# Kernel tuning notes

Measured on AMD Instinct MI355X. Metric: run time of the kernel, lower is better.

The kernel has to match this reference:

```python
import jax, jax.numpy as jnp
import numpy as np
import math

H, W, R = 100, 100, 2          # BEV grid and neighbor range
K = (2 * R + 1) ** 2           # 25 spatial neighbors
C = 256                        # input_dim == hidden_dim
NH, DK = 8, 32                 # heads, head dim
T = 5                          # temporal history length
NEG = -1e10                    # mask fill value from the source


def build_neighbors():
    # Clamped (2R+1)x(2R+1) window per pixel (faithful to the intent of
    # generate_spatial_neighbors: edge pixels reuse the nearest interior window).
    hs = np.clip(np.arange(H), R, H - 1 - R)
    ws = np.clip(np.arange(W), R, W - 1 - R)
    off = np.arange(-R, R + 1)
    rows = hs[:, None] + off[None, :]                      # [H, 2R+1]
    cols = ws[:, None] + off[None, :]                      # [W, 2R+1]
    idx = rows[:, None, :, None] * W + cols[None, :, None, :]  # [H,W,2R+1,2R+1]
    return idx.reshape(H * W, K).astype(np.int32)


def setup_inputs() -> dict:
    key = jax.random.key(0)
    ks = jax.random.split(key, 40)
    N = H * W
    inp = {"x": jax.random.normal(ks[0], (N, T, C), jnp.float32)}
    i = 1
    for pfx in ("t", "s"):
        for nm in ("q", "k", "v", "o"):
            inp[f"{pfx}_W{nm}"] = jax.random.normal(ks[i], (C, C), jnp.float32) * 0.02; i += 1
            inp[f"{pfx}_b{nm}"] = jax.random.normal(ks[i], (C,), jnp.float32) * 0.02; i += 1
    inp["neighbors"] = jnp.asarray(build_neighbors())
    inp["tmask"] = jnp.ones((N, 1, T), jnp.int32)
    inp["smask"] = jnp.ones((N, 1, K), jnp.int32)
    return inp


def _heads(x, Wx, b):
    # x: [N, L, C] -> [N, NH, L, DK]
    N, L, _ = x.shape
    return (x @ Wx + b).reshape(N, L, NH, DK).transpose(0, 2, 1, 3)


def _attend(q, k, v, mask4):
    # q: [N,NH,Lq,DK], k/v: [N,NH,Lk,DK], mask4: [N,1,1,Lk]
    scores = jnp.einsum('nhqd,nhkd->nhqk', q, k) / math.sqrt(q.shape[-1])
    scores = jnp.where(mask4 == 0, NEG, scores)
    p = jax.nn.softmax(scores, axis=-1)
    return jnp.einsum('nhqk,nhkd->nhqd', p, v)


def _forward(x, t_Wq, t_bq, t_Wk, t_bk, t_Wv, t_bv, t_Wo, t_bo,
             s_Wq, s_bq, s_Wk, s_bk, s_Wv, s_bv, s_Wo, s_bo,
             neighbors, tmask, smask):
    N = x.shape[0]
    # ---- temporal aggregation (MultiHeadedAttention): latest frame attends history
    q_last = x[:, -1:, :]                                   # [N,1,C]
    q = _heads(q_last, t_Wq, t_bq)                          # [N,NH,1,DK]
    k = _heads(x, t_Wk, t_bk)                               # [N,NH,T,DK]
    v = _heads(x, t_Wv, t_bv)
    ctx = _attend(q, k, v, tmask[:, None, :, :])            # [N,NH,1,DK]
    h_t = ctx.transpose(0, 2, 1, 3).reshape(N, 1, C) @ t_Wo + t_bo  # [N,1,C]
    # ---- spatial neighbor attention (MultiHeadedAttention_spatial):
    # K/V are projected from the query features, then gathered by neighbor index.
    sq = _heads(h_t, s_Wq, s_bq)                            # [N,NH,1,DK]
    k1 = h_t[:, 0, :] @ s_Wk + s_bk                          # [N,C] per-pixel key token
    v1 = h_t[:, 0, :] @ s_Wv + s_bv                          # [N,C]
    kn = k1[neighbors].reshape(N, K, NH, DK).transpose(0, 2, 1, 3)  # [N,NH,K,DK]
    vn = v1[neighbors].reshape(N, K, NH, DK).transpose(0, 2, 1, 3)
    sctx = _attend(sq, kn, vn, smask[:, None, :, :])        # [N,NH,1,DK]
    out = sctx.transpose(0, 2, 1, 3).reshape(N, 1, C) @ s_Wo + s_bo  # [N,1,C]
    return out


def reference(x, t_Wq, t_bq, t_Wk, t_bk, t_Wv, t_bv, t_Wo, t_bo,
              s_Wq, s_bq, s_Wk, s_bk, s_Wv, s_bv, s_Wo, s_bo,
              neighbors, tmask, smask):
    return _forward(x, t_Wq, t_bq, t_Wk, t_bk, t_Wv, t_bv, t_Wo, t_bo,
                    s_Wq, s_bq, s_Wk, s_bk, s_Wv, s_bv, s_Wo, s_bo,
                    neighbors, tmask, smask)
```

## Files before the change

kernel.cpp:

```cpp
#include <hip/hip_runtime.h>

constexpr int TT = 5;
constexpr int KK = 25;
#define NEGV -1e10f

typedef _Float16 f16;
typedef __attribute__((ext_vector_type(8))) _Float16 f16x8;
typedef __attribute__((ext_vector_type(4))) _Float16 f16x4;
typedef __attribute__((ext_vector_type(4))) float f32x4;

__device__ __forceinline__ void gload16(const void* g, void* l) {
    __builtin_amdgcn_global_load_lds(
        (const __attribute__((address_space(1))) unsigned int*)g,
        (__attribute__((address_space(3))) unsigned int*)l, 16, 0, 0);
}

__device__ __forceinline__ int xcd_remap(int id, int G) {
    const int c = id & 7, j = id >> 3;
    const int q = G >> 3, r = G & 7;
    const int base = (c < r) ? c * (q + 1) : r * (q + 1) + (c - r) * q;
    return base + j;
}

struct PrepArgs { const float* W[8]; const float* b[8]; };

__global__ __launch_bounds__(256) void prep_w8(
    PrepArgs pa, f16* __restrict__ wt, float* __restrict__ bc)
{
    __shared__ float sT[64][65];
    const int z = blockIdx.z;
    const float* W = pa.W[z];
    f16* wh = wt + (size_t)z * 65536;
    const int t  = threadIdx.x;
    const int k0 = blockIdx.x * 64, n0 = blockIdx.y * 64;
    const int kk = t >> 2;
    #pragma unroll
    for (int c = 0; c < 4; ++c) {
        const int col = (t & 3) * 16 + c * 4;
        float4 v = *(const float4*)(W + (size_t)(k0 + kk) * 256 + n0 + col);
        sT[kk][col] = v.x; sT[kk][col + 1] = v.y; sT[kk][col + 2] = v.z; sT[kk][col + 3] = v.w;
    }
    __syncthreads();
    const int n = t >> 2, ks = (t & 3) * 16;
    f16* ph = wh + (size_t)(n0 + n) * 256 + k0 + ks;
    #pragma unroll
    for (int j0 = 0; j0 < 16; j0 += 8) {
        f16x8 vh;
        #pragma unroll
        for (int j = 0; j < 8; ++j) vh[j] = (f16)sT[ks + j0 + j][n];
        *(f16x8*)(ph + j0) = vh;
    }
    if (blockIdx.x == 0 && blockIdx.y == 0) bc[z * 256 + t] = pa.b[z][t];
}

__global__ __launch_bounds__(256) void cvt_x(
    const float* __restrict__ x, f16* __restrict__ xh, int n8)
{
    for (int i = blockIdx.x * 256 + threadIdx.x; i < n8; i += gridDim.x * 256) {
        const float4 a = ((const float4*)x)[2 * i];
        const float4 b = ((const float4*)x)[2 * i + 1];
        f16x8 o;
        o[0] = (f16)a.x; o[1] = (f16)a.y; o[2] = (f16)a.z; o[3] = (f16)a.w;
        o[4] = (f16)b.x; o[5] = (f16)b.y; o[6] = (f16)b.z; o[7] = (f16)b.w;
        *(f16x8*)(xh + (size_t)i * 8) = o;
    }
}

template<int BM, int OM>
__global__ __launch_bounds__(512, 4) void gemm_f16(
    const f16* __restrict__ A, int lda, int M,
    const f16* __restrict__ W, const float* __restrict__ bias,
    float* __restrict__ Cf, f16* __restrict__ Ch, int ldc,
    int GY, int G)
{
    constexpr int MF   = BM / 32;
    constexpr int ASEG = BM / 64;
    __shared__ f16 sA[2][BM * 64];
    __shared__ f16 sB[2][128 * 64];

    const int tid = threadIdx.x;
    const int l   = tid & 63, w = tid >> 6;
    const int l15 = l & 15, l4 = l >> 4;
    const int wm  = w >> 2, wn = w & 3;

    const int p  = xcd_remap(blockIdx.x, G);
    const int bm = (p / GY) * BM;
    const int bn = (p % GY) * 128;

    const int srow8 = l >> 3;
    const int scol  = ((l & 7) ^ srow8) * 8;
    size_t aoff[ASEG];
    #pragma unroll
    for (int j = 0; j < ASEG; ++j) {
        int r = bm + (w * ASEG + j) * 8 + srow8;
        if (r > M - 1) r = M - 1;
        aoff[j] = (size_t)r * lda + scol;
    }
    size_t boff[2];
    #pragma unroll
    for (int j = 0; j < 2; ++j)
        boff[j] = (size_t)(bn + (w * 2 + j) * 8 + srow8) * 256 + scol;

    f32x4 acc[MF][2];
    #pragma unroll
    for (int i = 0; i < MF; ++i)
        #pragma unroll
        for (int j = 0; j < 2; ++j) acc[i][j] = f32x4{0.f, 0.f, 0.f, 0.f};

    auto STAGE = [&](int buf, int k0) {
        #pragma unroll
        for (int j = 0; j < ASEG; ++j)
            gload16(A + aoff[j] + k0, &sA[buf][(w * ASEG + j) * 512]);
        #pragma unroll
        for (int j = 0; j < 2; ++j)
            gload16(W + boff[j] + k0, &sB[buf][(w * 2 + j) * 512]);
    };

    STAGE(0, 0);
    __syncthreads();

    const int swz = l15 & 7;
    #pragma unroll
    for (int t = 0; t < 4; ++t) {
        if (t < 3) STAGE((t + 1) & 1, (t + 1) * 64);

        f16x8 af[MF][2], bf[2][2];
        #pragma unroll
        for (int mf = 0; mf < MF; ++mf) {
            const int r = wm * (BM / 2) + mf * 16 + l15;
            #pragma unroll
            for (int ks = 0; ks < 2; ++ks)
                af[mf][ks] = *(const f16x8*)&sA[t & 1][r * 64 + (((ks * 4 + l4) ^ swz) * 8)];
        }
        #pragma unroll
        for (int nf = 0; nf < 2; ++nf) {
            const int r = wn * 32 + nf * 16 + l15;
            #pragma unroll
            for (int ks = 0; ks < 2; ++ks)
                bf[nf][ks] = *(const f16x8*)&sB[t & 1][r * 64 + (((ks * 4 + l4) ^ swz) * 8)];
        }
        #pragma unroll
        for (int mf = 0; mf < MF; ++mf)
            #pragma unroll
            for (int nf = 0; nf < 2; ++nf)
                #pragma unroll
                for (int ks = 0; ks < 2; ++ks)
                    acc[mf][nf] = __builtin_amdgcn_mfma_f32_16x16x32_f16(
                        af[mf][ks], bf[nf][ks], acc[mf][nf], 0, 0, 0);
        __syncthreads();
    }

    #pragma unroll
    for (int mf = 0; mf < MF; ++mf) {
        const int row0 = bm + wm * (BM / 2) + mf * 16 + l4 * 4;
        #pragma unroll
        for (int nf = 0; nf < 2; ++nf) {
            const int col = bn + wn * 32 + nf * 16 + l15;
            const float bs = bias[col];
            #pragma unroll
            for (int i = 0; i < 4; ++i) {
                const int row = row0 + i;
                if (row < M) {
                    const float v = acc[mf][nf][i] + bs;
                    const size_t o = (size_t)row * ldc + col;
                    if (OM == 0) Cf[o] = v;
                    else         Ch[o] = (f16)v;
                }
            }
        }
    }
}

__global__ __launch_bounds__(256) void attn_t(
    const f16* __restrict__ q, const f16* __restrict__ kv,
    const int* __restrict__ tmask, f16* __restrict__ ctx)
{
    const int tid = threadIdx.x;
    const int wv = tid >> 6, l = tid & 63;
    const int n = blockIdx.x * 4 + wv;
    const int col = ((l >> 3) * 32) + (l & 7) * 4;
    const float scale = 0.1767766952966369f;

    const f16x4 qv = *(const f16x4*)(q + (size_t)n * 256 + col);
    const float q0 = (float)qv[0], q1 = (float)qv[1], q2 = (float)qv[2], q3 = (float)qv[3];

    float m = -3.0e38f, lsum = 0.f;
    float a0 = 0.f, a1 = 0.f, a2 = 0.f, a3 = 0.f;
    #pragma unroll
    for (int t = 0; t < TT; ++t) {
        const size_t row = ((size_t)n * TT + t) * 512;
        const f16x4 kk = *(const f16x4*)(kv + row + col);
        const f16x4 vv = *(const f16x4*)(kv + row + 256 + col);
        float p = q0 * (float)kk[0] + q1 * (float)kk[1]
                + q2 * (float)kk[2] + q3 * (float)kk[3];
        p += __shfl_xor(p, 1);
        p += __shfl_xor(p, 2);
        p += __shfl_xor(p, 4);
        const float s  = (tmask[n * TT + t] == 0) ? NEGV : p * scale;
        const float mn = fmaxf(m, s);
        const float sc = exp2f((m - mn) * 1.44269504f);
        const float pe = exp2f((s - mn) * 1.44269504f);
        lsum = lsum * sc + pe;
        a0 = a0 * sc + pe * (float)vv[0];
        a1 = a1 * sc + pe * (float)vv[1];
        a2 = a2 * sc + pe * (float)vv[2];
        a3 = a3 * sc + pe * (float)vv[3];
        m = mn;
    }
    const float inv = 1.0f / lsum;
    f16x4 o;
    o[0] = (f16)(a0 * inv); o[1] = (f16)(a1 * inv);
    o[2] = (f16)(a2 * inv); o[3] = (f16)(a3 * inv);
    *(f16x4*)(ctx + (size_t)n * 256 + col) = o;
}

__global__ __launch_bounds__(256) void attn_s(
    const f16* __restrict__ sqkv, const int* __restrict__ nbrs,
    const int* __restrict__ smask, f16* __restrict__ sctx, int G)
{
    __shared__ int nbL[4 * KK];
    __shared__ int mkL[4 * KK];
    const int tid = threadIdx.x;
    const int nbase = xcd_remap(blockIdx.x, G) * 4;
    if (tid < 4 * KK) {
        nbL[tid] = nbrs[nbase * KK + tid];
        mkL[tid] = smask[nbase * KK + tid];
    }
    __syncthreads();

    const int wv = tid >> 6, l = tid & 63;
    const int n = nbase + wv;
    const int col = ((l >> 3) * 32) + (l & 7) * 4;
    const float scale = 0.1767766952966369f;

    const f16x4 qv = *(const f16x4*)(sqkv + (size_t)n * 768 + col);
    const float q0 = (float)qv[0], q1 = (float)qv[1], q2 = (float)qv[2], q3 = (float)qv[3];

    float m = -3.0e38f, lsum = 0.f;
    float a0 = 0.f, a1 = 0.f, a2 = 0.f, a3 = 0.f;
    #pragma unroll
    for (int j = 0; j < KK; ++j) {
        const size_t row = (size_t)nbL[wv * KK + j] * 768;
        const f16x4 kk = *(const f16x4*)(sqkv + row + 256 + col);
        const f16x4 vv = *(const f16x4*)(sqkv + row + 512 + col);
        float p = q0 * (float)kk[0] + q1 * (float)kk[1]
                + q2 * (float)kk[2] + q3 * (float)kk[3];
        p += __shfl_xor(p, 1);
        p += __shfl_xor(p, 2);
        p += __shfl_xor(p, 4);
        const float s  = (mkL[wv * KK + j] == 0) ? NEGV : p * scale;
        const float mn = fmaxf(m, s);
        const float sc = exp2f((m - mn) * 1.44269504f);
        const float pe = exp2f((s - mn) * 1.44269504f);
        lsum = lsum * sc + pe;
        a0 = a0 * sc + pe * (float)vv[0];
        a1 = a1 * sc + pe * (float)vv[1];
        a2 = a2 * sc + pe * (float)vv[2];
        a3 = a3 * sc + pe * (float)vv[3];
        m = mn;
    }
    const float inv = 1.0f / lsum;
    f16x4 o;
    o[0] = (f16)(a0 * inv); o[1] = (f16)(a1 * inv);
    o[2] = (f16)(a2 * inv); o[3] = (f16)(a3 * inv);
    *(f16x4*)(sctx + (size_t)n * 256 + col) = o;
}

extern "C" void kernel_launch(void* const* d_in, const int* in_sizes, int n_in,
                              void* d_out, int out_size, void* d_ws, size_t ws_size,
                              hipStream_t stream)
{
    const float* x = (const float*)d_in[0];
    const int* nbrs  = (const int*)d_in[17];
    const int* tmask = (const int*)d_in[18];
    const int* smask = (const int*)d_in[19];
    float* out = (float*)d_out;

    const int N  = in_sizes[0] / (TT * 256);
    const int MT = N * TT;

    f16* wt  = (f16*)d_ws;
    float* bc = (float*)(wt + (size_t)2048 * 256);
    f16* xh     = (f16*)(bc + 2048);
    f16* kvbuf  = xh + (size_t)MT * 256;
    f16* q16    = kvbuf + (size_t)MT * 512;
    f16* ctx    = q16 + (size_t)N * 256;
    f16* ht     = ctx + (size_t)N * 256;
    f16* sqkv16 = ht + (size_t)N * 256;
    f16* sctx   = sqkv16 + (size_t)N * 768;

    PrepArgs pa;
    pa.W[0] = (const float*)d_in[3];  pa.b[0] = (const float*)d_in[4];
    pa.W[1] = (const float*)d_in[5];  pa.b[1] = (const float*)d_in[6];
    pa.W[2] = (const float*)d_in[1];  pa.b[2] = (const float*)d_in[2];
    pa.W[3] = (const float*)d_in[7];  pa.b[3] = (const float*)d_in[8];
    pa.W[4] = (const float*)d_in[9];  pa.b[4] = (const float*)d_in[10];
    pa.W[5] = (const float*)d_in[11]; pa.b[5] = (const float*)d_in[12];
    pa.W[6] = (const float*)d_in[13]; pa.b[6] = (const float*)d_in[14];
    pa.W[7] = (const float*)d_in[15]; pa.b[7] = (const float*)d_in[16];
    prep_w8<<<dim3(4, 4, 8), 256, 0, stream>>>(pa, wt, bc);

    cvt_x<<<2048, 256, 0, stream>>>(x, xh, MT * 256 / 8);

    dim3 blk(512);
    const int GBM_T = (MT + 127) / 128;
    const int GBM_S = (N + 63) / 64;

    gemm_f16<128, 1><<<GBM_T * 4, blk, 0, stream>>>(
        xh, 256, MT, wt, bc, nullptr, kvbuf, 512, 4, GBM_T * 4);
    gemm_f16<64, 1><<<GBM_S * 2, blk, 0, stream>>>(
        xh + (TT - 1) * 256, TT * 256, N,
        wt + (size_t)512 * 256, bc + 512, nullptr, q16, 256, 2, GBM_S * 2);
    attn_t<<<N / 4, dim3(256), 0, stream>>>(q16, kvbuf, tmask, ctx);
    gemm_f16<64, 1><<<GBM_S * 2, blk, 0, stream>>>(
        ctx, 256, N, wt + (size_t)768 * 256, bc + 768,
        nullptr, ht, 256, 2, GBM_S * 2);
    gemm_f16<64, 1><<<GBM_S * 6, blk, 0, stream>>>(
        ht, 256, N, wt + (size_t)1024 * 256, bc + 1024,
        nullptr, sqkv16, 768, 6, GBM_S * 6);
    attn_s<<<N / 4, dim3(256), 0, stream>>>(sqkv16, nbrs, smask, sctx, N / 4);
    gemm_f16<64, 0><<<GBM_S * 2, blk, 0, stream>>>(
        sctx, 256, N, wt + (size_t)1792 * 256, bc + 1792,
        out, nullptr, 256, 2, GBM_S * 2);
}
```

Measured before the change: 227.1 us.

## Fold temporal output projection into spatial QKV weights and batch kernel launches

Precomputes the product of the temporal output projection and the spatial Q/K/V weights (plus the folded bias) inside the prep kernel, which removes the h_t GEMM and its intermediate buffer. Weight prep and x conversion are merged into one launch, and the KV and Q projection GEMMs share a single launch through a two-job dispatch. All GEMMs now use 128-row tiles. This cuts two launches and one full GEMM pass, in exchange for a small fp32 weight-product GEMM each call and different fp16 rounding of the combined weights.

```diff
diff --git a/kernel.cpp b/kernel.cpp
--- a/kernel.cpp
+++ b/kernel.cpp
@@ -22,60 +22,111 @@
     return base + j;
 }
 
-struct PrepArgs { const float* W[8]; const float* b[8]; };
-
-__global__ __launch_bounds__(256) void prep_w8(
-    PrepArgs pa, f16* __restrict__ wt, float* __restrict__ bc)
-{
-    __shared__ float sT[64][65];
-    const int z = blockIdx.z;
-    const float* W = pa.W[z];
-    f16* wh = wt + (size_t)z * 65536;
-    const int t  = threadIdx.x;
-    const int k0 = blockIdx.x * 64, n0 = blockIdx.y * 64;
-    const int kk = t >> 2;
-    #pragma unroll
-    for (int c = 0; c < 4; ++c) {
-        const int col = (t & 3) * 16 + c * 4;
-        float4 v = *(const float4*)(W + (size_t)(k0 + kk) * 256 + n0 + col);
-        sT[kk][col] = v.x; sT[kk][col + 1] = v.y; sT[kk][col + 2] = v.z; sT[kk][col + 3] = v.w;
-    }
-    __syncthreads();
-    const int n = t >> 2, ks = (t & 3) * 16;
-    f16* ph = wh + (size_t)(n0 + n) * 256 + k0 + ks;
-    #pragma unroll
-    for (int j0 = 0; j0 < 16; j0 += 8) {
-        f16x8 vh;
-        #pragma unroll
-        for (int j = 0; j < 8; ++j) vh[j] = (f16)sT[ks + j0 + j][n];
-        *(f16x8*)(ph + j0) = vh;
-    }
-    if (blockIdx.x == 0 && blockIdx.y == 0) bc[z * 256 + t] = pa.b[z][t];
-}
-
-__global__ __launch_bounds__(256) void cvt_x(
+struct PrepAll {
+    const float* Wt[4]; const float* bt[4];
+    const float* tWo;   const float* tbo;
+    const float* sW[3]; const float* sb[3];
+};
+
+__global__ __launch_bounds__(256) void prep_all(
+    PrepAll pp, f16* __restrict__ wt, float* __restrict__ bc,
+    f16* __restrict__ wc, float* __restrict__ bcs,
     const float* __restrict__ x, f16* __restrict__ xh, int n8)
 {
-    for (int i = blockIdx.x * 256 + threadIdx.x; i < n8; i += gridDim.x * 256) {
-        const float4 a = ((const float4*)x)[2 * i];
-        const float4 b = ((const float4*)x)[2 * i + 1];
-        f16x8 o;
-        o[0] = (f16)a.x; o[1] = (f16)a.y; o[2] = (f16)a.z; o[3] = (f16)a.w;
-        o[4] = (f16)b.x; o[5] = (f16)b.y; o[6] = (f16)b.z; o[7] = (f16)b.w;
-        *(f16x8*)(xh + (size_t)i * 8) = o;
-    }
-}
-
-template<int BM, int OM>
-__global__ __launch_bounds__(512, 4) void gemm_f16(
-    const f16* __restrict__ A, int lda, int M,
-    const f16* __restrict__ W, const float* __restrict__ bias,
-    float* __restrict__ Cf, f16* __restrict__ Ch, int ldc,
-    int GY, int G)
-{
-    constexpr int MF   = BM / 32;
-    constexpr int ASEG = BM / 64;
-    __shared__ f16 sA[2][BM * 64];
+    const int bid = blockIdx.x, t = threadIdx.x;
+
+    if (bid < 64) {
+        __shared__ float sT[64][65];
+        const int z = bid >> 4, sub = bid & 15;
+        const int k0 = (sub >> 2) * 64, n0 = (sub & 3) * 64;
+        const float* W = pp.Wt[z];
+        f16* wh = wt + (size_t)z * 65536;
+        const int kk = t >> 2;
+        #pragma unroll
+        for (int c = 0; c < 4; ++c) {
+            const int col = (t & 3) * 16 + c * 4;
+            float4 v = *(const float4*)(W + (size_t)(k0 + kk) * 256 + n0 + col);
+            sT[kk][col] = v.x; sT[kk][col + 1] = v.y;
+            sT[kk][col + 2] = v.z; sT[kk][col + 3] = v.w;
+        }
+        __syncthreads();
+        const int n = t >> 2, ks = (t & 3) * 16;
+        f16* ph = wh + (size_t)(n0 + n) * 256 + k0 + ks;
+        #pragma unroll
+        for (int j0 = 0; j0 < 16; j0 += 8) {
+            f16x8 vh;
+            #pragma unroll
+            for (int j = 0; j < 8; ++j) vh[j] = (f16)sT[ks + j0 + j][n];
+            *(f16x8*)(ph + j0) = vh;
+        }
+        if (sub == 0) bc[z * 256 + t] = pp.bt[z][t];
+    } else if (bid < 112) {
+        const int cb = bid - 64;
+        const int m0 = (cb / 12) * 64;
+        const int nt = cb % 12;
+        const int sel = nt >> 2;
+        const int nc0 = (nt & 3) * 64;
+        const float* Amat = pp.tWo;
+        const float* Bmat = pp.sW[sel];
+        __shared__ float sa[16][68];
+        __shared__ float sbm[16][64];
+        const int tm = t >> 4, tn = t & 15;
+        const int r = t >> 2, cA = (t & 3) << 2;
+        const int kB = t >> 4, jB = (t & 15) << 2;
+        float acc[4][4] = {};
+        for (int c0 = 0; c0 < 256; c0 += 16) {
+            float4 a4 = *(const float4*)(Amat + (size_t)(m0 + r) * 256 + c0 + cA);
+            float4 b4 = *(const float4*)(Bmat + (size_t)(c0 + kB) * 256 + nc0 + jB);
+            __syncthreads();
+            sa[cA + 0][r] = a4.x; sa[cA + 1][r] = a4.y;
+            sa[cA + 2][r] = a4.z; sa[cA + 3][r] = a4.w;
+            *(float4*)(&sbm[kB][jB]) = b4;
+            __syncthreads();
+            #pragma unroll
+            for (int k = 0; k < 16; ++k) {
+                float4 a = *(const float4*)(&sa[k][tm * 4]);
+                float4 b = *(const float4*)(&sbm[k][tn * 4]);
+                acc[0][0] += a.x * b.x; acc[0][1] += a.x * b.y; acc[0][2] += a.x * b.z; acc[0][3] += a.x * b.w;
+                acc[1][0] += a.y * b.x; acc[1][1] += a.y * b.y; acc[1][2] += a.y * b.z; acc[1][3] += a.y * b.w;
+                acc[2][0] += a.z * b.x; acc[2][1] += a.z * b.y; acc[2][2] += a.z * b.z; acc[2][3] += a.z * b.w;
+                acc[3][0] += a.w * b.x; acc[3][1] += a.w * b.y; acc[3][2] += a.w * b.z; acc[3][3] += a.w * b.w;
+            }
+        }
+        const int ng0 = nt * 64 + tn * 4;
+        #pragma unroll
+        for (int i = 0; i < 4; ++i)
+            #pragma unroll
+            for (int j = 0; j < 4; ++j)
+                wc[(size_t)(ng0 + j) * 256 + m0 + tm * 4 + i] = (f16)acc[i][j];
+    } else if (bid == 112) {
+        #pragma unroll
+        for (int rgn = 0; rgn < 3; ++rgn) {
+            const float* B = pp.sW[rgn];
+            float a = 0.f;
+            for (int c = 0; c < 256; ++c) a += pp.tbo[c] * B[(size_t)c * 256 + t];
+            bcs[rgn * 256 + t] = a + pp.sb[rgn][t];
+        }
+    } else {
+        for (int i = (bid - 113) * 256 + t; i < n8; i += 2048 * 256) {
+            const float4 a = ((const float4*)x)[2 * i];
+            const float4 b = ((const float4*)x)[2 * i + 1];
+            f16x8 o;
+            o[0] = (f16)a.x; o[1] = (f16)a.y; o[2] = (f16)a.z; o[3] = (f16)a.w;
+            o[4] = (f16)b.x; o[5] = (f16)b.y; o[6] = (f16)b.z; o[7] = (f16)b.w;
+            *(f16x8*)(xh + (size_t)i * 8) = o;
+        }
+    }
+}
+
+struct GJob {
+    const f16* A; const f16* W; const float* bias;
+    f16* C16; float* C32;
+    int lda, M, ldc, GY, nblk;
+};
+
+__global__ __launch_bounds__(512, 4) void gemm_f16(GJob j0, GJob j1, int G)
+{
+    __shared__ f16 sA[2][128 * 64];
     __shared__ f16 sB[2][128 * 64];
 
     const int tid = threadIdx.x;
@@ -83,37 +134,41 @@
     const int l15 = l & 15, l4 = l >> 4;
     const int wm  = w >> 2, wn = w & 3;
 
-    const int p  = xcd_remap(blockIdx.x, G);
-    const int bm = (p / GY) * BM;
-    const int bn = (p % GY) * 128;
+    int p = xcd_remap(blockIdx.x, G);
+    const bool first = (p < j0.nblk);
+    const GJob jb = first ? j0 : j1;
+    if (!first) p -= j0.nblk;
+
+    const int bm = (p / jb.GY) * 128;
+    const int bn = (p % jb.GY) * 128;
 
     const int srow8 = l >> 3;
     const int scol  = ((l & 7) ^ srow8) * 8;
-    size_t aoff[ASEG];
-    #pragma unroll
-    for (int j = 0; j < ASEG; ++j) {
-        int r = bm + (w * ASEG + j) * 8 + srow8;
-        if (r > M - 1) r = M - 1;
-        aoff[j] = (size_t)r * lda + scol;
+    size_t aoff[2];
+    #pragma unroll
+    for (int j = 0; j < 2; ++j) {
+        int r = bm + (w * 2 + j) * 8 + srow8;
+        if (r > jb.M - 1) r = jb.M - 1;
+        aoff[j] = (size_t)r * jb.lda + scol;
     }
     size_t boff[2];
     #pragma unroll
     for (int j = 0; j < 2; ++j)
         boff[j] = (size_t)(bn + (w * 2 + j) * 8 + srow8) * 256 + scol;
 
-    f32x4 acc[MF][2];
-    #pragma unroll
-    for (int i = 0; i < MF; ++i)
+    f32x4 acc[4][2];
+    #pragma unroll
+    for (int i = 0; i < 4; ++i)
         #pragma unroll
         for (int j = 0; j < 2; ++j) acc[i][j] = f32x4{0.f, 0.f, 0.f, 0.f};
 
     auto STAGE = [&](int buf, int k0) {
         #pragma unroll
-        for (int j = 0; j < ASEG; ++j)
-            gload16(A + aoff[j] + k0, &sA[buf][(w * ASEG + j) * 512]);
-        #pragma unroll
         for (int j = 0; j < 2; ++j)
-            gload16(W + boff[j] + k0, &sB[buf][(w * 2 + j) * 512]);
+            gload16(jb.A + aoff[j] + k0, &sA[buf][(w * 2 + j) * 512]);
+        #pragma unroll
+        for (int j = 0; j < 2; ++j)
+            gload16(jb.W + boff[j] + k0, &sB[buf][(w * 2 + j) * 512]);
     };
 
     STAGE(0, 0);
@@ -124,10 +179,10 @@
     for (int t = 0; t < 4; ++t) {
         if (t < 3) STAGE((t + 1) & 1, (t + 1) * 64);
 
-        f16x8 af[MF][2], bf[2][2];
-        #pragma unroll
-        for (int mf = 0; mf < MF; ++mf) {
-            const int r = wm * (BM / 2) + mf * 16 + l15;
+        f16x8 af[4][2], bf[2][2];
+        #pragma unroll
+        for (int mf = 0; mf < 4; ++mf) {
+            const int r = wm * 64 + mf * 16 + l15;
             #pragma unroll
             for (int ks = 0; ks < 2; ++ks)
                 af[mf][ks] = *(const f16x8*)&sA[t & 1][r * 64 + (((ks * 4 + l4) ^ swz) * 8)];
@@ -140,7 +195,7 @@
                 bf[nf][ks] = *(const f16x8*)&sB[t & 1][r * 64 + (((ks * 4 + l4) ^ swz) * 8)];
         }
         #pragma unroll
-        for (int mf = 0; mf < MF; ++mf)
+        for (int mf = 0; mf < 4; ++mf)
             #pragma unroll
             for (int nf = 0; nf < 2; ++nf)
                 #pragma unroll
@@ -151,20 +206,20 @@
     }
 
     #pragma unroll
-    for (int mf = 0; mf < MF; ++mf) {
-        const int row0 = bm + wm * (BM / 2) + mf * 16 + l4 * 4;
+    for (int mf = 0; mf < 4; ++mf) {
+        const int row0 = bm + wm * 64 + mf * 16 + l4 * 4;
         #pragma unroll
         for (int nf = 0; nf < 2; ++nf) {
             const int col = bn + wn * 32 + nf * 16 + l15;
-            const float bs = bias[col];
+            const float bs = jb.bias[col];
             #pragma unroll
             for (int i = 0; i < 4; ++i) {
                 const int row = row0 + i;
-                if (row < M) {
+                if (row < jb.M) {
                     const float v = acc[mf][nf][i] + bs;
-                    const size_t o = (size_t)row * ldc + col;
-                    if (OM == 0) Cf[o] = v;
-                    else         Ch[o] = (f16)v;
+                    const size_t o = (size_t)row * jb.ldc + col;
+                    if (jb.C32) jb.C32[o] = v;
+                    else        jb.C16[o] = (f16)v;
                 }
             }
         }
@@ -280,46 +335,41 @@
     const int MT = N * TT;
 
     f16* wt  = (f16*)d_ws;
-    float* bc = (float*)(wt + (size_t)2048 * 256);
-    f16* xh     = (f16*)(bc + 2048);
+    f16* wc  = wt + (size_t)1024 * 256;
+    float* bc  = (float*)(wc + (size_t)768 * 256);
+    float* bcs = bc + 1024;
+    f16* xh     = (f16*)(bcs + 768);
     f16* kvbuf  = xh + (size_t)MT * 256;
     f16* q16    = kvbuf + (size_t)MT * 512;
     f16* ctx    = q16 + (size_t)N * 256;
-    f16* ht     = ctx + (size_t)N * 256;
-    f16* sqkv16 = ht + (size_t)N * 256;
+    f16* sqkv16 = ctx + (size_t)N * 256;
     f16* sctx   = sqkv16 + (size_t)N * 768;
 
-    PrepArgs pa;
-    pa.W[0] = (const float*)d_in[3];  pa.b[0] = (const float*)d_in[4];
-    pa.W[1] = (const float*)d_in[5];  pa.b[1] = (const float*)d_in[6];
-    pa.W[2] = (const float*)d_in[1];  pa.b[2] = (const float*)d_in[2];
-    pa.W[3] = (const float*)d_in[7];  pa.b[3] = (const float*)d_in[8];
-    pa.W[4] = (const float*)d_in[9];  pa.b[4] = (const float*)d_in[10];
-    pa.W[5] = (const float*)d_in[11]; pa.b[5] = (const float*)d_in[12];
-    pa.W[6] = (const float*)d_in[13]; pa.b[6] = (const float*)d_in[14];
-    pa.W[7] = (const float*)d_in[15]; pa.b[7] = (const float*)d_in[16];
-    prep_w8<<<dim3(4, 4, 8), 256, 0, stream>>>(pa, wt, bc);
-
-    cvt_x<<<2048, 256, 0, stream>>>(x, xh, MT * 256 / 8);
-
-    dim3 blk(512);
+    PrepAll pp;
+    pp.Wt[0] = (const float*)d_in[3];  pp.bt[0] = (const float*)d_in[4];
+    pp.Wt[1] = (const float*)d_in[5];  pp.bt[1] = (const float*)d_in[6];
+    pp.Wt[2] = (const float*)d_in[1];  pp.bt[2] = (const float*)d_in[2];
+    pp.Wt[3] = (const float*)d_in[15]; pp.bt[3] = (const float*)d_in[16];
+    pp.tWo   = (const float*)d_in[7];  pp.tbo   = (const float*)d_in[8];
+    pp.sW[0] = (const float*)d_in[9];  pp.sb[0] = (const float*)d_in[10];
+    pp.sW[1] = (const float*)d_in[11]; pp.sb[1] = (const float*)d_in[12];
+    pp.sW[2] = (const float*)d_in[13]; pp.sb[2] = (const float*)d_in[14];
+
+    prep_all<<<113 + 2048, 256, 0, stream>>>(pp, wt, bc, wc, bcs, x, xh, MT * 256 / 8);
+
     const int GBM_T = (MT + 127) / 128;
-    const int GBM_S = (N + 63) / 64;
-
-    gemm_f16<128, 1><<<GBM_T * 4, blk, 0, stream>>>(
-        xh, 256, MT, wt, bc, nullptr, kvbuf, 512, 4, GBM_T * 4);
-    gemm_f16<64, 1><<<GBM_S * 2, blk, 0, stream>>>(
-        xh + (TT - 1) * 256, TT * 256, N,
-        wt + (size_t)512 * 256, bc + 512, nullptr, q16, 256, 2, GBM_S * 2);
-    attn_t<<<N / 4, dim3(256), 0, stream>>>(q16, kvbuf, tmask, ctx);
-    gemm_f16<64, 1><<<GBM_S * 2, blk, 0, stream>>>(
-        ctx, 256, N, wt + (size_t)768 * 256, bc + 768,
-        nullptr, ht, 256, 2, GBM_S * 2);
-    gemm_f16<64, 1><<<GBM_S * 6, blk, 0, stream>>>(
-        ht, 256, N, wt + (size_t)1024 * 256, bc + 1024,
-        nullptr, sqkv16, 768, 6, GBM_S * 6);
-    attn_s<<<N / 4, dim3(256), 0, stream>>>(sqkv16, nbrs, smask, sctx, N / 4);
-    gemm_f16<64, 0><<<GBM_S * 2, blk, 0, stream>>>(
-        sctx, 256, N, wt + (size_t)1792 * 256, bc + 1792,
-        out, nullptr, 256, 2, GBM_S * 2);
-}
+    const int GBM_N = (N + 127) / 128;
+
+    GJob jkv  = { xh, wt, bc, kvbuf, nullptr, 256, MT, 512, 4, GBM_T * 4 };
+    GJob jq   = { xh + 4 * 256, wt + (size_t)512 * 256, bc + 512,
+                  q16, nullptr, TT * 256, N, 256, 2, GBM_N * 2 };
+    GJob jsq  = { ctx, wc, bcs, sqkv16, nullptr, 256, N, 768, 6, GBM_N * 6 };
+    GJob jout = { sctx, wt + (size_t)768 * 256, bc + 768,
+                  nullptr, out, 256, N, 256, 2, GBM_N * 2 };
+
+    gemm_f16<<<jkv.nblk + jq.nblk, 512, 0, stream>>>(jkv, jq, jkv.nblk + jq.nblk);
+    attn_t<<<N / 4, 256, 0, stream>>>(q16, kvbuf, tmask, ctx);
+    gemm_f16<<<jsq.nblk, 512, 0, stream>>>(jsq, jsq, jsq.nblk);
+    attn_s<<<N / 4, 256, 0, stream>>>(sqkv16, nbrs, smask, sctx, N / 4);
+    gemm_f16<<<jout.nblk, 512, 0, stream>>>(jout, jout, jout.nblk);
+}
```

Result: slower. 237.4 us (+4.5%).
